# Performance work log

Measured on AMD Instinct MI355X. Metric: run time of the kernel, lower is better.

The kernel has to match this reference:

```python
import jax, jax.numpy as jnp
import numpy as np

B, N, T, D, H, E = 2, 1024, 8, 128, 4, 8192
DH = D // H
NEG_SLOPE = 0.2  # GATv2Conv default negative_slope


def _ln(x, g, b):
    m = jnp.mean(x, -1, keepdims=True)
    v = jnp.mean((x - m) ** 2, -1, keepdims=True)
    return (x - m) * jax.lax.rsqrt(v + 1e-5) * g + b


def _forward(x, edge_index, gat_wl, gat_wr, gat_att, gat_b, in_w, in_b, out_w, out_b,
             ffn_w1, ffn_b1, ffn_w2, ffn_b2, fus_w, fus_b,
             lns_g, lns_b, lnt1_g, lnt1_b, lnt2_g, lnt2_b, lnf_g, lnf_b):
    # ---- spatial branch: GATv2, vectorized over (B, T) instead of python loops ----
    loops = jnp.arange(N)
    src = jnp.concatenate([edge_index[0], loops])  # j: message source (PyG adds self loops)
    dst = jnp.concatenate([edge_index[1], loops])  # i: aggregation target
    xl = jnp.einsum('bntd,de->bnte', x, gat_wl).reshape(B, N, T, H, D)
    xr = jnp.einsum('bntd,de->bnte', x, gat_wr).reshape(B, N, T, H, D)
    ml = xl[:, src]                                  # [B,Et,T,H,D]
    mr = xr[:, dst]
    e = jax.nn.leaky_relu(ml + mr, NEG_SLOPE)
    logits = jnp.einsum('bethd,hd->beth', e, gat_att)
    logits = jnp.moveaxis(logits, 1, 0)              # [Et,B,T,H]
    mx = jax.ops.segment_max(logits, dst, num_segments=N)
    p = jnp.exp(logits - mx[dst])                    # stable edge softmax per dst node
    ssum = jax.ops.segment_sum(p, dst, num_segments=N)
    alpha = p / ssum[dst]                            # [Et,B,T,H]
    msg = alpha[..., None] * jnp.moveaxis(ml, 1, 0)
    agg = jax.ops.segment_sum(msg, dst, num_segments=N)  # [N,B,T,H,D]
    x_sp = jnp.moveaxis(agg.mean(3), 0, 1) + gat_b   # concat=False -> head mean; [B,N,T,D]
    x_sp = _ln(x_sp, lns_g, lns_b)

    # ---- temporal branch: MHA + FFN, vectorized over all B*N nodes ----
    xt = x.reshape(B * N, T, D)
    qkv = xt @ in_w + in_b
    q, k, v = jnp.split(qkv, 3, axis=-1)
    q = q.reshape(B * N, T, H, DH)
    k = k.reshape(B * N, T, H, DH)
    v = v.reshape(B * N, T, H, DH)
    scores = jnp.einsum('bthd,bshd->bhts', q, k) / np.float32(np.sqrt(DH))
    attn = jax.nn.softmax(scores, -1)
    o = jnp.einsum('bhts,bshd->bthd', attn, v).reshape(B * N, T, D)
    o = o @ out_w + out_b
    x1 = _ln(xt + o, lnt1_g, lnt1_b)
    ffn = jax.nn.gelu(x1 @ ffn_w1 + ffn_b1, approximate=False) @ ffn_w2 + ffn_b2
    x_tp = _ln(x1 + ffn, lnt2_g, lnt2_b).reshape(B, N, T, D)

    # ---- gated fusion with residual ----
    g = jax.nn.sigmoid(jnp.concatenate([x_sp, x_tp], -1) @ fus_w + fus_b)
    return _ln(g * x_sp + (1.0 - g) * x_tp + x, lnf_g, lnf_b)


def setup_inputs() -> dict:
    key = jax.random.key(0)
    ks = jax.random.split(key, 12)
    s = 0.05
    f = jnp.float32
    return {
        'x': jax.random.normal(ks[0], (B, N, T, D), f),
        'edge_index': jax.random.randint(ks[1], (2, E), 0, N),
        'gat_wl': jax.random.normal(ks[2], (D, H * D), f) * s,
        'gat_wr': jax.random.normal(ks[3], (D, H * D), f) * s,
        'gat_att': jax.random.normal(ks[4], (H, D), f) * s,
        'gat_b': jnp.zeros((D,), f),
        'in_w': jax.random.normal(ks[5], (D, 3 * D), f) * s,
        'in_b': jnp.zeros((3 * D,), f),
        'out_w': jax.random.normal(ks[6], (D, D), f) * s,
        'out_b': jnp.zeros((D,), f),
        'ffn_w1': jax.random.normal(ks[7], (D, 4 * D), f) * s,
        'ffn_b1': jnp.zeros((4 * D,), f),
        'ffn_w2': jax.random.normal(ks[8], (4 * D, D), f) * s,
        'ffn_b2': jnp.zeros((D,), f),
        'fus_w': jax.random.normal(ks[9], (2 * D, D), f) * s,
        'fus_b': jnp.zeros((D,), f),
        'lns_g': jnp.ones((D,), f), 'lns_b': jnp.zeros((D,), f),
        'lnt1_g': jnp.ones((D,), f), 'lnt1_b': jnp.zeros((D,), f),
        'lnt2_g': jnp.ones((D,), f), 'lnt2_b': jnp.zeros((D,), f),
        'lnf_g': jnp.ones((D,), f), 'lnf_b': jnp.zeros((D,), f),
    }


def reference(x, edge_index, gat_wl, gat_wr, gat_att, gat_b, in_w, in_b, out_w, out_b,
              ffn_w1, ffn_b1, ffn_w2, ffn_b2, fus_w, fus_b,
              lns_g, lns_b, lnt1_g, lnt1_b, lnt2_g, lnt2_b, lnf_g, lnf_b):
    return _forward(x, edge_index, gat_wl, gat_wr, gat_att, gat_b, in_w, in_b, out_w, out_b,
                    ffn_w1, ffn_b1, ffn_w2, ffn_b2, fus_w, fus_b,
                    lns_g, lns_b, lnt1_g, lnt1_b, lnt2_g, lnt2_b, lnf_g, lnf_b)
```

## Files before the change

kernel.cpp:

```cpp
#include <hip/hip_runtime.h>
#include <math.h>

#define B_ 2
#define N_ 1024
#define T_ 8
#define D_ 128
#define H_ 4
#define E_ 8192
#define EN_ 9216
#define M_ 16384

typedef unsigned short u16;
using bf16x8 = __attribute__((ext_vector_type(8))) short;
using f32x4  = __attribute__((ext_vector_type(4))) float;

__device__ __forceinline__ float bf2f(unsigned int u) {
  return __uint_as_float(u << 16);
}
__device__ __forceinline__ u16 f2bf(float f) {
  unsigned int x = __float_as_uint(f);
  x += 0x7fffu + ((x >> 16) & 1u);
  return (u16)(x >> 16);
}
__device__ __forceinline__ void load8f(const u16* p, float* f) {
  uint4 u = *(const uint4*)p;
  f[0]=bf2f(u.x & 0xffffu); f[1]=bf2f(u.x >> 16);
  f[2]=bf2f(u.y & 0xffffu); f[3]=bf2f(u.y >> 16);
  f[4]=bf2f(u.z & 0xffffu); f[5]=bf2f(u.z >> 16);
  f[6]=bf2f(u.w & 0xffffu); f[7]=bf2f(u.w >> 16);
}
__device__ __forceinline__ void gl2lds(const u16* g, u16* l) {
  __builtin_amdgcn_global_load_lds(
      (const __attribute__((address_space(1))) unsigned int*)(const void*)g,
      (__attribute__((address_space(3))) unsigned int*)(void*)l,
      16, 0, 0);
}

__global__ __launch_bounds__(256) void prep_k(const float* __restrict__ x,
                                              const float* __restrict__ wl,
                                              const float* __restrict__ wr,
                                              const float* __restrict__ inw,
                                              const float* __restrict__ outw,
                                              const float* __restrict__ f1,
                                              const float* __restrict__ f2,
                                              const float* __restrict__ fw,
                                              u16* __restrict__ XB,
                                              u16* __restrict__ WB) {
  int bi = blockIdx.x;
  if (bi < 2048) {
    int i = (bi * 256 + threadIdx.x) * 4;
    float4 v = *(const float4*)&x[i];
    u16 o[4] = {f2bf(v.x), f2bf(v.y), f2bf(v.z), f2bf(v.w)};
    *(ushort4*)&XB[i] = *(ushort4*)o;
    return;
  }
  int idx = (bi - 2048) * 256 + threadIdx.x;
  const float* src; int base, K, N;
  if      (idx < 65536)  { src = wl;   base = 0;      K = 128; N = 512; }
  else if (idx < 131072) { src = wr;   base = 65536;  K = 128; N = 512; }
  else if (idx < 180224) { src = inw;  base = 131072; K = 128; N = 384; }
  else if (idx < 196608) { src = outw; base = 180224; K = 128; N = 128; }
  else if (idx < 262144) { src = f1;   base = 196608; K = 128; N = 512; }
  else if (idx < 327680) { src = f2;   base = 262144; K = 512; N = 128; }
  else                   { src = fw;   base = 327680; K = 256; N = 128; }
  int o = idx - base;
  int n = o / K, k = o - n * K;
  WB[idx] = f2bf(src[k * N + n]);
}

__global__ __launch_bounds__(1024) void csr_k(const int* __restrict__ ei,
                                              int* __restrict__ offs,
                                              int* __restrict__ eids) {
  __shared__ int cnt[N_];
  __shared__ int cur[N_];
  int tid = threadIdx.x;
  cnt[tid] = 0;
  __syncthreads();
  for (int e = tid; e < EN_; e += 1024) {
    int d = (e < E_) ? ei[E_ + e] : (e - E_);
    atomicAdd(&cnt[d], 1);
  }
  __syncthreads();
  int mine = cnt[tid];
  for (int off = 1; off < 1024; off <<= 1) {
    int tv = (tid >= off) ? cnt[tid - off] : 0;
    __syncthreads();
    cnt[tid] += tv;
    __syncthreads();
  }
  int excl = cnt[tid] - mine;
  offs[tid] = excl;
  if (tid == 1023) offs[N_] = cnt[1023];
  cur[tid] = excl;
  __syncthreads();
  for (int e = tid; e < EN_; e += 1024) {
    int d = (e < E_) ? ei[E_ + e] : (e - E_);
    int pos = atomicAdd(&cur[d], 1);
    eids[pos] = e;
  }
}

template<int BM, int ACT, int ROUTE>
__global__ __launch_bounds__(256) void gemm_k(const u16* __restrict__ A, int lda,
                                              const u16* __restrict__ WT, int K,
                                              const float* __restrict__ bias,
                                              u16* __restrict__ C, int ldc,
                                              u16* __restrict__ R0,
                                              u16* __restrict__ R1,
                                              u16* __restrict__ R2,
                                              const float* __restrict__ b2) {
  constexpr int MI = BM / 32;
  __shared__ u16 As[BM * 32];
  __shared__ u16 Bs[128 * 32];
  int tid = threadIdx.x;
  int bx = blockIdx.x, by = blockIdx.y;
  int lane = tid & 63, wid = tid >> 6;
  int lr = lane & 15, lk = lane >> 4;
  int wm = (wid >> 1) * (BM / 2);
  int wn = (wid & 1) * 64;

  u16* Cb; int ldc_; int col0; const float* bias_;
  if (ROUTE) {
    if (bx < 4)      { Cb = R0; ldc_ = 512; col0 = bx * 128;       bias_ = nullptr; }
    else if (bx < 8) { Cb = R1; ldc_ = 512; col0 = (bx - 4) * 128; bias_ = nullptr; }
    else             { Cb = R2; ldc_ = 384; col0 = (bx - 8) * 128; bias_ = b2; }
  } else { Cb = C; ldc_ = ldc; col0 = bx * 128; bias_ = bias; }

  f32x4 acc[MI][4] = {};
  for (int k0 = 0; k0 < K; k0 += 32) {
    __syncthreads();
#pragma unroll
    for (int i = 0; i < BM / 64; ++i) {
      int o = tid * 16 + i * 4096;
      int row = o >> 6;
      int col = (o >> 1) & 31;
      gl2lds(A + (size_t)(by * BM + row) * lda + k0 + col,
             (u16*)((char*)As + wid * 1024 + i * 4096));
    }
#pragma unroll
    for (int i = 0; i < 2; ++i) {
      int o = tid * 16 + i * 4096;
      int nrow = o >> 6;
      int col = (o >> 1) & 31;
      gl2lds(WT + (size_t)(bx * 128 + nrow) * K + k0 + col,
             (u16*)((char*)Bs + wid * 1024 + i * 4096));
    }
    __syncthreads();
    bf16x8 bf[4];
#pragma unroll
    for (int ni = 0; ni < 4; ++ni)
      bf[ni] = *(const bf16x8*)&Bs[(wn + ni * 16 + lr) * 32 + lk * 8];
#pragma unroll
    for (int mi = 0; mi < MI; ++mi) {
      bf16x8 af = *(const bf16x8*)&As[(wm + mi * 16 + lr) * 32 + lk * 8];
#pragma unroll
      for (int ni = 0; ni < 4; ++ni)
        acc[mi][ni] = __builtin_amdgcn_mfma_f32_16x16x32_bf16(af, bf[ni], acc[mi][ni], 0, 0, 0);
    }
  }
  float bc[4];
#pragma unroll
  for (int ni = 0; ni < 4; ++ni)
    bc[ni] = bias_ ? bias_[col0 + wn + ni * 16 + lr] : 0.f;
#pragma unroll
  for (int mi = 0; mi < MI; ++mi) {
#pragma unroll
    for (int r = 0; r < 4; ++r) {
      int row = by * BM + wm + mi * 16 + lk * 4 + r;
#pragma unroll
      for (int ni = 0; ni < 4; ++ni) {
        int col = col0 + wn + ni * 16 + lr;
        float v = acc[mi][ni][r] + bc[ni];
        if (ACT) v = 0.5f * v * (1.f + erff(v * 0.70710678118f));
        Cb[(size_t)row * ldc_ + col] = f2bf(v);
      }
    }
  }
}

template<int EPI>
__global__ __launch_bounds__(256) void gemm_ln_k(const u16* __restrict__ A, int lda,
                                                 const u16* __restrict__ WT, int K,
                                                 const float* __restrict__ bias,
                                                 const float* __restrict__ xres,
                                                 const float* __restrict__ xsp,
                                                 const float* __restrict__ xtp,
                                                 const float* __restrict__ lng,
                                                 const float* __restrict__ lnb,
                                                 float* __restrict__ o32,
                                                 u16* __restrict__ o16, int os16) {
  __shared__ u16 As[64 * 32];
  __shared__ u16 Bs[128 * 32];
  __shared__ float rs[64][2], rq[64][2];
  int tid = threadIdx.x;
  int by = blockIdx.y;
  int lane = tid & 63, wid = tid >> 6;
  int lr = lane & 15, lk = lane >> 4;
  int wm = (wid >> 1) * 32, wn = (wid & 1) * 64;

  f32x4 acc[2][4] = {};
  for (int k0 = 0; k0 < K; k0 += 32) {
    __syncthreads();
    {
      int o = tid * 16;
      int row = o >> 6;
      int col = (o >> 1) & 31;
      gl2lds(A + (size_t)(by * 64 + row) * lda + k0 + col,
             (u16*)((char*)As + wid * 1024));
    }
#pragma unroll
    for (int i = 0; i < 2; ++i) {
      int o = tid * 16 + i * 4096;
      int nrow = o >> 6;
      int col = (o >> 1) & 31;
      gl2lds(WT + (size_t)nrow * K + k0 + col,
             (u16*)((char*)Bs + wid * 1024 + i * 4096));
    }
    __syncthreads();
    bf16x8 bf[4];
#pragma unroll
    for (int ni = 0; ni < 4; ++ni)
      bf[ni] = *(const bf16x8*)&Bs[(wn + ni * 16 + lr) * 32 + lk * 8];
#pragma unroll
    for (int mi = 0; mi < 2; ++mi) {
      bf16x8 af = *(const bf16x8*)&As[(wm + mi * 16 + lr) * 32 + lk * 8];
#pragma unroll
      for (int ni = 0; ni < 4; ++ni)
        acc[mi][ni] = __builtin_amdgcn_mfma_f32_16x16x32_bf16(af, bf[ni], acc[mi][ni], 0, 0, 0);
    }
  }
  float bc[4];
#pragma unroll
  for (int ni = 0; ni < 4; ++ni) bc[ni] = bias[wn + ni * 16 + lr];

#pragma unroll
  for (int mi = 0; mi < 2; ++mi) {
#pragma unroll
    for (int r = 0; r < 4; ++r) {
      int row = by * 64 + wm + mi * 16 + lk * 4 + r;
      float s = 0.f, s2 = 0.f;
#pragma unroll
      for (int ni = 0; ni < 4; ++ni) {
        int col = wn + ni * 16 + lr;
        float v = acc[mi][ni][r] + bc[ni];
        if (EPI == 1 || EPI == 2) {
          v += xres[(size_t)row * 128 + col];
        } else {
          float gg = 1.f / (1.f + expf(-v));
          v = gg * xsp[(size_t)row * 128 + col] + (1.f - gg) * xtp[(size_t)row * 128 + col]
              + xres[(size_t)row * 128 + col];
        }
        acc[mi][ni][r] = v;
        s += v; s2 += v * v;
      }
      s += __shfl_xor(s, 1, 64); s2 += __shfl_xor(s2, 1, 64);
      s += __shfl_xor(s, 2, 64); s2 += __shfl_xor(s2, 2, 64);
      s += __shfl_xor(s, 4, 64); s2 += __shfl_xor(s2, 4, 64);
      s += __shfl_xor(s, 8, 64); s2 += __shfl_xor(s2, 8, 64);
      if (lr == 0) {
        int rl = wm + mi * 16 + lk * 4 + r;
        rs[rl][wid & 1] = s;
        rq[rl][wid & 1] = s2;
      }
    }
  }
  __syncthreads();
#pragma unroll
  for (int mi = 0; mi < 2; ++mi) {
#pragma unroll
    for (int r = 0; r < 4; ++r) {
      int rl = wm + mi * 16 + lk * 4 + r;
      int row = by * 64 + rl;
      float tot = rs[rl][0] + rs[rl][1];
      float tq = rq[rl][0] + rq[rl][1];
      float mean = tot * (1.f / 128.f);
      float var = tq * (1.f / 128.f) - mean * mean;
      float rinv = rsqrtf(var + 1e-5f);
#pragma unroll
      for (int ni = 0; ni < 4; ++ni) {
        int col = wn + ni * 16 + lr;
        float o = (acc[mi][ni][r] - mean) * rinv * lng[col] + lnb[col];
        o32[(size_t)row * 128 + col] = o;
        if (EPI != 3) o16[(size_t)row * os16 + col] = f2bf(o);
      }
    }
  }
}

__global__ __launch_bounds__(64) void gat_fused_k(const u16* __restrict__ XL,
                                                  const u16* __restrict__ XR,
                                                  const int* __restrict__ offs,
                                                  const int* __restrict__ eids,
                                                  const int* __restrict__ ei,
                                                  const float* __restrict__ att,
                                                  const float* __restrict__ gb,
                                                  const float* __restrict__ lng,
                                                  const float* __restrict__ lnb,
                                                  float* __restrict__ XSP,
                                                  u16* __restrict__ XCAT) {
  int bid = blockIdx.x;
  int n = bid >> 4;
  int b = (bid >> 3) & 1;
  int t = bid & 7;
  int lane = threadIdx.x;
  int dd = (lane & 15) * 8;
  size_t tokn = (size_t)(b * N_ + n) * 8 + t;

  float mr[8], av[8];
  load8f(XR + tokn * 512 + lane * 8, mr);
  *(float4*)&av[0] = *(const float4*)(att + lane * 8);
  *(float4*)&av[4] = *(const float4*)(att + lane * 8 + 4);

  int beg = offs[n], end = offs[n + 1];
  float mH = -1e30f, sH = 0.f;
  float acc[8] = {0.f, 0.f, 0.f, 0.f, 0.f, 0.f, 0.f, 0.f};
  for (int i = beg; i < end; ++i) {
    int e = eids[i];
    int src = (e < E_) ? ei[e] : (e - E_);
    float ml[8];
    load8f(XL + ((size_t)(b * N_ + src) * 8 + t) * 512 + lane * 8, ml);
    float d = 0.f;
#pragma unroll
    for (int j = 0; j < 8; ++j) {
      float m = ml[j] + mr[j];
      m = (m > 0.f) ? m : 0.2f * m;
      d += m * av[j];
    }
    d += __shfl_xor(d, 1, 64);
    d += __shfl_xor(d, 2, 64);
    d += __shfl_xor(d, 4, 64);
    d += __shfl_xor(d, 8, 64);
    float mNew = fmaxf(mH, d);
    float scale = expf(mH - mNew);
    float p = expf(d - mNew);
    sH = sH * scale + p;
#pragma unroll
    for (int j = 0; j < 8; ++j) acc[j] = acc[j] * scale + p * ml[j];
    mH = mNew;
  }
  float invS = 1.f / sH;
#pragma unroll
  for (int j = 0; j < 8; ++j) acc[j] *= invS;
#pragma unroll
  for (int j = 0; j < 8; ++j) {
    acc[j] += __shfl_xor(acc[j], 16, 64);
    acc[j] += __shfl_xor(acc[j], 32, 64);
  }
#pragma unroll
  for (int j = 0; j < 8; ++j) acc[j] = acc[j] * 0.25f + gb[dd + j];
  float s = 0.f, s2 = 0.f;
#pragma unroll
  for (int j = 0; j < 8; ++j) { s += acc[j]; s2 += acc[j] * acc[j]; }
#pragma unroll
  for (int m = 1; m < 16; m <<= 1) {
    s += __shfl_xor(s, m, 64);
    s2 += __shfl_xor(s2, m, 64);
  }
  float mean = s * (1.f / 128.f);
  float var = s2 * (1.f / 128.f) - mean * mean;
  float r = rsqrtf(var + 1e-5f);
  if (lane < 16) {
    float o[8];
    u16 ob[8];
#pragma unroll
    for (int j = 0; j < 8; ++j) {
      o[j] = (acc[j] - mean) * r * lng[dd + j] + lnb[dd + j];
      ob[j] = f2bf(o[j]);
    }
    *(float4*)(XSP + tokn * 128 + dd)     = *(float4*)&o[0];
    *(float4*)(XSP + tokn * 128 + dd + 4) = *(float4*)&o[4];
    *(uint4*)&XCAT[tokn * 256 + dd] = *(uint4*)ob;
  }
}

__global__ __launch_bounds__(256) void attn_k(const u16* __restrict__ QKV,
                                              u16* __restrict__ OATT) {
  int pair = blockIdx.x * 4 + (threadIdx.x >> 6);
  int lane = threadIdx.x & 63;
  int bn = pair >> 2, h = pair & 3;
  int t = lane >> 3, s = lane & 7;
  const u16* base = QKV + (size_t)bn * 8 * 384;
  const u16* qp = base + t * 384 + h * 32;
  const u16* kp = base + s * 384 + 128 + h * 32;
  float sc = 0.f;
#pragma unroll
  for (int d0 = 0; d0 < 32; d0 += 8) {
    float q[8], k[8];
    load8f(qp + d0, q);
    load8f(kp + d0, k);
#pragma unroll
    for (int j = 0; j < 8; ++j) sc += q[j] * k[j];
  }
  sc *= 0.17677669529663687f;
  float m = sc;
  m = fmaxf(m, __shfl_xor(m, 1, 64));
  m = fmaxf(m, __shfl_xor(m, 2, 64));
  m = fmaxf(m, __shfl_xor(m, 4, 64));
  float p = expf(sc - m);
  float S = p;
  S += __shfl_xor(S, 1, 64);
  S += __shfl_xor(S, 2, 64);
  S += __shfl_xor(S, 4, 64);
  float alpha = p / S;
  int dg = lane & 7;
  int tbase = lane & 56;
  float o0 = 0.f, o1 = 0.f, o2 = 0.f, o3 = 0.f;
#pragma unroll
  for (int s2 = 0; s2 < 8; ++s2) {
    float a = __shfl(alpha, tbase + s2, 64);
    const u16* vp = base + s2 * 384 + 256 + h * 32 + dg * 4;
    o0 += a * bf2f(vp[0]);
    o1 += a * bf2f(vp[1]);
    o2 += a * bf2f(vp[2]);
    o3 += a * bf2f(vp[3]);
  }
  u16 ov[4] = {f2bf(o0), f2bf(o1), f2bf(o2), f2bf(o3)};
  *(ushort4*)&OATT[((size_t)bn * 8 + t) * 128 + h * 32 + dg * 4] = *(ushort4*)ov;
}

extern "C" void kernel_launch(void* const* d_in, const int* in_sizes, int n_in,
                              void* d_out, int out_size, void* d_ws, size_t ws_size,
                              hipStream_t stream) {
  const float* x       = (const float*)d_in[0];
  const int*   ei      = (const int*)d_in[1];
  const float* gat_att = (const float*)d_in[4];
  const float* gat_b   = (const float*)d_in[5];
  const float* in_b    = (const float*)d_in[7];
  const float* out_b   = (const float*)d_in[9];
  const float* ffn_b1  = (const float*)d_in[11];
  const float* ffn_b2  = (const float*)d_in[13];
  const float* fus_b   = (const float*)d_in[15];
  const float* lns_g   = (const float*)d_in[16];
  const float* lns_b   = (const float*)d_in[17];
  const float* lnt1_g  = (const float*)d_in[18];
  const float* lnt1_b  = (const float*)d_in[19];
  const float* lnt2_g  = (const float*)d_in[20];
  const float* lnt2_b  = (const float*)d_in[21];
  const float* lnf_g   = (const float*)d_in[22];
  const float* lnf_b   = (const float*)d_in[23];

  char* ws = (char*)d_ws;
  u16*   WB    = (u16*)ws;
  u16*   WT1   = WB;
  u16*   WTO   = WB + 180224;
  u16*   WTF1  = WB + 196608;
  u16*   WTF2  = WB + 262144;
  u16*   WTFUS = WB + 327680;
  int*   OFFS  = (int*)(ws + 3145728);
  int*   EIDS  = (int*)(ws + 3153920);
  u16*   XB   = (u16*)(ws + 4194304);
  u16*   OATT = XB;
  u16*   XL   = (u16*)(ws + 8388608);
  u16*   FFNH = XL;
  u16*   XR   = (u16*)(ws + 25165824);
  float* X1   = (float*)(ws + 33554432);
  u16*   QKV  = (u16*)(ws + 41943040);
  u16*   X1B  = (u16*)(ws + 41943040);
  float* XSP  = (float*)(ws + 54525952);
  u16*   XCAT = (u16*)(ws + 62914560);
  float* XTP  = (float*)(ws + 71303168);

  prep_k<<<dim3(3456), dim3(256), 0, stream>>>(x,
      (const float*)d_in[2], (const float*)d_in[3], (const float*)d_in[6],
      (const float*)d_in[8], (const float*)d_in[10], (const float*)d_in[12],
      (const float*)d_in[14], XB, WB);
  csr_k<<<dim3(1), dim3(1024), 0, stream>>>(ei, OFFS, EIDS);

  gemm_k<128,0,1><<<dim3(11, 128), dim3(256), 0, stream>>>(
      XB, 128, WT1, 128, nullptr, nullptr, 0, XL, XR, QKV, in_b);

  gat_fused_k<<<dim3(16384), dim3(64), 0, stream>>>(XL, XR, OFFS, EIDS, ei,
      gat_att, gat_b, lns_g, lns_b, XSP, XCAT);

  attn_k<<<dim3(2048), dim3(256), 0, stream>>>(QKV, OATT);
  gemm_ln_k<1><<<dim3(1, 256), dim3(256), 0, stream>>>(
      OATT, 128, WTO, 128, out_b, x, nullptr, nullptr, lnt1_g, lnt1_b, X1, X1B, 128);
  gemm_k<128,1,0><<<dim3(4, 128), dim3(256), 0, stream>>>(
      X1B, 128, WTF1, 128, ffn_b1, FFNH, 512, nullptr, nullptr, nullptr, nullptr);
  gemm_ln_k<2><<<dim3(1, 256), dim3(256), 0, stream>>>(
      FFNH, 512, WTF2, 512, ffn_b2, X1, nullptr, nullptr, lnt2_g, lnt2_b,
      XTP, XCAT + 128, 256);

  gemm_ln_k<3><<<dim3(1, 256), dim3(256), 0, stream>>>(
      XCAT, 256, WTFUS, 256, fus_b, x, XSP, XTP, lnf_g, lnf_b,
      (float*)d_out, nullptr, 0);
}
```

Baseline: 241.1 us.

## Merge prep with CSR build, fuse GAT with temporal attention, drop fp32 intermediates

Folds weight/input conversion and CSR construction into one launch, and runs the GAT aggregation and the temporal MHA as separate block ranges of a single kernel. The fp32 XSP/XTP buffers are removed, so the fusion epilogue reads the bf16 spatial and temporal branch values from XCAT. This cuts launch count and memory traffic, at the cost of lower precision in the gating inputs. The single CSR block now sits in a 601-block grid, which may leave it as a late straggler.

```diff
diff --git a/kernel.cpp b/kernel.cpp
--- a/kernel.cpp
+++ b/kernel.cpp
@@ -36,25 +36,9 @@
       16, 0, 0);
 }
 
-__global__ __launch_bounds__(256) void prep_k(const float* __restrict__ x,
-                                              const float* __restrict__ wl,
-                                              const float* __restrict__ wr,
-                                              const float* __restrict__ inw,
-                                              const float* __restrict__ outw,
-                                              const float* __restrict__ f1,
-                                              const float* __restrict__ f2,
-                                              const float* __restrict__ fw,
-                                              u16* __restrict__ XB,
-                                              u16* __restrict__ WB) {
-  int bi = blockIdx.x;
-  if (bi < 2048) {
-    int i = (bi * 256 + threadIdx.x) * 4;
-    float4 v = *(const float4*)&x[i];
-    u16 o[4] = {f2bf(v.x), f2bf(v.y), f2bf(v.z), f2bf(v.w)};
-    *(ushort4*)&XB[i] = *(ushort4*)o;
-    return;
-  }
-  int idx = (bi - 2048) * 256 + threadIdx.x;
+__device__ __forceinline__ u16 conv_w_elem(int idx,
+    const float* wl, const float* wr, const float* inw, const float* outw,
+    const float* f1, const float* f2, const float* fw) {
   const float* src; int base, K, N;
   if      (idx < 65536)  { src = wl;   base = 0;      K = 128; N = 512; }
   else if (idx < 131072) { src = wr;   base = 65536;  K = 128; N = 512; }
@@ -65,15 +49,34 @@
   else                   { src = fw;   base = 327680; K = 256; N = 128; }
   int o = idx - base;
   int n = o / K, k = o - n * K;
-  WB[idx] = f2bf(src[k * N + n]);
-}
-
-__global__ __launch_bounds__(1024) void csr_k(const int* __restrict__ ei,
-                                              int* __restrict__ offs,
-                                              int* __restrict__ eids) {
+  return f2bf(src[k * N + n]);
+}
+
+__global__ __launch_bounds__(1024) void prep_csr_k(const float* __restrict__ x,
+    const float* __restrict__ wl, const float* __restrict__ wr,
+    const float* __restrict__ inw, const float* __restrict__ outw,
+    const float* __restrict__ f1, const float* __restrict__ f2,
+    const float* __restrict__ fw,
+    u16* __restrict__ XB, u16* __restrict__ WB,
+    const int* __restrict__ ei, int* __restrict__ offs, int* __restrict__ eids) {
   __shared__ int cnt[N_];
   __shared__ int cur[N_];
+  int bi = blockIdx.x;
   int tid = threadIdx.x;
+  if (bi < 512) {
+    int i = (bi * 1024 + tid) * 4;
+    float4 v = *(const float4*)&x[i];
+    u16 o[4] = {f2bf(v.x), f2bf(v.y), f2bf(v.z), f2bf(v.w)};
+    *(ushort4*)&XB[i] = *(ushort4*)o;
+    return;
+  }
+  if (bi < 600) {
+    int base = (bi - 512) * 4096 + tid * 4;
+#pragma unroll
+    for (int j = 0; j < 4; ++j)
+      WB[base + j] = conv_w_elem(base + j, wl, wr, inw, outw, f1, f2, fw);
+    return;
+  }
   cnt[tid] = 0;
   __syncthreads();
   for (int e = tid; e < EN_; e += 1024) {
@@ -183,8 +186,7 @@
                                                  const u16* __restrict__ WT, int K,
                                                  const float* __restrict__ bias,
                                                  const float* __restrict__ xres,
-                                                 const float* __restrict__ xsp,
-                                                 const float* __restrict__ xtp,
+                                                 const u16* __restrict__ xcat,
                                                  const float* __restrict__ lng,
                                                  const float* __restrict__ lnb,
                                                  float* __restrict__ o32,
@@ -247,8 +249,9 @@
           v += xres[(size_t)row * 128 + col];
         } else {
           float gg = 1.f / (1.f + expf(-v));
-          v = gg * xsp[(size_t)row * 128 + col] + (1.f - gg) * xtp[(size_t)row * 128 + col]
-              + xres[(size_t)row * 128 + col];
+          float xsp = bf2f(xcat[(size_t)row * 256 + col]);
+          float xtp = bf2f(xcat[(size_t)row * 256 + 128 + col]);
+          v = gg * xsp + (1.f - gg) * xtp + xres[(size_t)row * 128 + col];
         }
         acc[mi][ni][r] = v;
         s += v; s2 += v * v;
@@ -280,14 +283,14 @@
       for (int ni = 0; ni < 4; ++ni) {
         int col = wn + ni * 16 + lr;
         float o = (acc[mi][ni][r] - mean) * rinv * lng[col] + lnb[col];
-        o32[(size_t)row * 128 + col] = o;
+        if (EPI != 2) o32[(size_t)row * 128 + col] = o;
         if (EPI != 3) o16[(size_t)row * os16 + col] = f2bf(o);
       }
     }
   }
 }
 
-__global__ __launch_bounds__(64) void gat_fused_k(const u16* __restrict__ XL,
+__global__ __launch_bounds__(256) void gat_attn_k(const u16* __restrict__ XL,
                                                   const u16* __restrict__ XR,
                                                   const int* __restrict__ offs,
                                                   const int* __restrict__ eids,
@@ -296,92 +299,88 @@
                                                   const float* __restrict__ gb,
                                                   const float* __restrict__ lng,
                                                   const float* __restrict__ lnb,
-                                                  float* __restrict__ XSP,
-                                                  u16* __restrict__ XCAT) {
+                                                  u16* __restrict__ XCAT,
+                                                  const u16* __restrict__ QKV,
+                                                  u16* __restrict__ OATT) {
   int bid = blockIdx.x;
-  int n = bid >> 4;
-  int b = (bid >> 3) & 1;
-  int t = bid & 7;
-  int lane = threadIdx.x;
-  int dd = (lane & 15) * 8;
-  size_t tokn = (size_t)(b * N_ + n) * 8 + t;
-
-  float mr[8], av[8];
-  load8f(XR + tokn * 512 + lane * 8, mr);
-  *(float4*)&av[0] = *(const float4*)(att + lane * 8);
-  *(float4*)&av[4] = *(const float4*)(att + lane * 8 + 4);
-
-  int beg = offs[n], end = offs[n + 1];
-  float mH = -1e30f, sH = 0.f;
-  float acc[8] = {0.f, 0.f, 0.f, 0.f, 0.f, 0.f, 0.f, 0.f};
-  for (int i = beg; i < end; ++i) {
-    int e = eids[i];
-    int src = (e < E_) ? ei[e] : (e - E_);
-    float ml[8];
-    load8f(XL + ((size_t)(b * N_ + src) * 8 + t) * 512 + lane * 8, ml);
-    float d = 0.f;
+  int wid = threadIdx.x >> 6;
+  int lane = threadIdx.x & 63;
+  if (bid < 4096) {
+    int w = bid * 4 + wid;
+    int n = w >> 4;
+    int b = (w >> 3) & 1;
+    int t = w & 7;
+    int dd = (lane & 15) * 8;
+    size_t tokn = (size_t)(b * N_ + n) * 8 + t;
+
+    float mr[8], av[8];
+    load8f(XR + tokn * 512 + lane * 8, mr);
+    *(float4*)&av[0] = *(const float4*)(att + lane * 8);
+    *(float4*)&av[4] = *(const float4*)(att + lane * 8 + 4);
+
+    int beg = offs[n], end = offs[n + 1];
+    float mH = -1e30f, sH = 0.f;
+    float acc[8] = {0.f, 0.f, 0.f, 0.f, 0.f, 0.f, 0.f, 0.f};
+    for (int i = beg; i < end; ++i) {
+      int e = eids[i];
+      int src = (e < E_) ? ei[e] : (e - E_);
+      float ml[8];
+      load8f(XL + ((size_t)(b * N_ + src) * 8 + t) * 512 + lane * 8, ml);
+      float d = 0.f;
+#pragma unroll
+      for (int j = 0; j < 8; ++j) {
+        float m = ml[j] + mr[j];
+        m = (m > 0.f) ? m : 0.2f * m;
+        d += m * av[j];
+      }
+      d += __shfl_xor(d, 1, 64);
+      d += __shfl_xor(d, 2, 64);
+      d += __shfl_xor(d, 4, 64);
+      d += __shfl_xor(d, 8, 64);
+      float mNew = fmaxf(mH, d);
+      float scale = expf(mH - mNew);
+      float p = expf(d - mNew);
+      sH = sH * scale + p;
+#pragma unroll
+      for (int j = 0; j < 8; ++j) acc[j] = acc[j] * scale + p * ml[j];
+      mH = mNew;
+    }
+    float invS = 1.f / sH;
+#pragma unroll
+    for (int j = 0; j < 8; ++j) acc[j] *= invS;
 #pragma unroll
     for (int j = 0; j < 8; ++j) {
-      float m = ml[j] + mr[j];
-      m = (m > 0.f) ? m : 0.2f * m;
-      d += m * av[j];
-    }
-    d += __shfl_xor(d, 1, 64);
-    d += __shfl_xor(d, 2, 64);
-    d += __shfl_xor(d, 4, 64);
-    d += __shfl_xor(d, 8, 64);
-    float mNew = fmaxf(mH, d);
-    float scale = expf(mH - mNew);
-    float p = expf(d - mNew);
-    sH = sH * scale + p;
-#pragma unroll
-    for (int j = 0; j < 8; ++j) acc[j] = acc[j] * scale + p * ml[j];
-    mH = mNew;
-  }
-  float invS = 1.f / sH;
-#pragma unroll
-  for (int j = 0; j < 8; ++j) acc[j] *= invS;
-#pragma unroll
-  for (int j = 0; j < 8; ++j) {
-    acc[j] += __shfl_xor(acc[j], 16, 64);
-    acc[j] += __shfl_xor(acc[j], 32, 64);
-  }
-#pragma unroll
-  for (int j = 0; j < 8; ++j) acc[j] = acc[j] * 0.25f + gb[dd + j];
-  float s = 0.f, s2 = 0.f;
-#pragma unroll
-  for (int j = 0; j < 8; ++j) { s += acc[j]; s2 += acc[j] * acc[j]; }
-#pragma unroll
-  for (int m = 1; m < 16; m <<= 1) {
-    s += __shfl_xor(s, m, 64);
-    s2 += __shfl_xor(s2, m, 64);
-  }
-  float mean = s * (1.f / 128.f);
-  float var = s2 * (1.f / 128.f) - mean * mean;
-  float r = rsqrtf(var + 1e-5f);
-  if (lane < 16) {
-    float o[8];
-    u16 ob[8];
-#pragma unroll
-    for (int j = 0; j < 8; ++j) {
-      o[j] = (acc[j] - mean) * r * lng[dd + j] + lnb[dd + j];
-      ob[j] = f2bf(o[j]);
-    }
-    *(float4*)(XSP + tokn * 128 + dd)     = *(float4*)&o[0];
-    *(float4*)(XSP + tokn * 128 + dd + 4) = *(float4*)&o[4];
-    *(uint4*)&XCAT[tokn * 256 + dd] = *(uint4*)ob;
-  }
-}
-
-__global__ __launch_bounds__(256) void attn_k(const u16* __restrict__ QKV,
-                                              u16* __restrict__ OATT) {
-  int pair = blockIdx.x * 4 + (threadIdx.x >> 6);
-  int lane = threadIdx.x & 63;
+      acc[j] += __shfl_xor(acc[j], 16, 64);
+      acc[j] += __shfl_xor(acc[j], 32, 64);
+    }
+#pragma unroll
+    for (int j = 0; j < 8; ++j) acc[j] = acc[j] * 0.25f + gb[dd + j];
+    float s = 0.f, s2 = 0.f;
+#pragma unroll
+    for (int j = 0; j < 8; ++j) { s += acc[j]; s2 += acc[j] * acc[j]; }
+#pragma unroll
+    for (int m = 1; m < 16; m <<= 1) {
+      s += __shfl_xor(s, m, 64);
+      s2 += __shfl_xor(s2, m, 64);
+    }
+    float mean = s * (1.f / 128.f);
+    float var = s2 * (1.f / 128.f) - mean * mean;
+    float r = rsqrtf(var + 1e-5f);
+    if (lane < 16) {
+      u16 ob[8];
+#pragma unroll
+      for (int j = 0; j < 8; ++j)
+        ob[j] = f2bf((acc[j] - mean) * r * lng[dd + j] + lnb[dd + j]);
+      *(uint4*)&XCAT[tokn * 256 + dd] = *(uint4*)ob;
+    }
+    return;
+  }
+  int pair = (bid - 4096) * 4 + wid;
   int bn = pair >> 2, h = pair & 3;
-  int t = lane >> 3, s = lane & 7;
+  int t = lane >> 3, sidx = lane & 7;
   const u16* base = QKV + (size_t)bn * 8 * 384;
   const u16* qp = base + t * 384 + h * 32;
-  const u16* kp = base + s * 384 + 128 + h * 32;
+  const u16* kp = base + sidx * 384 + 128 + h * 32;
   float sc = 0.f;
 #pragma unroll
   for (int d0 = 0; d0 < 32; d0 += 8) {
@@ -456,32 +455,30 @@
   float* X1   = (float*)(ws + 33554432);
   u16*   QKV  = (u16*)(ws + 41943040);
   u16*   X1B  = (u16*)(ws + 41943040);
-  float* XSP  = (float*)(ws + 54525952);
   u16*   XCAT = (u16*)(ws + 62914560);
-  float* XTP  = (float*)(ws + 71303168);
-
-  prep_k<<<dim3(3456), dim3(256), 0, stream>>>(x,
+
+  prep_csr_k<<<dim3(601), dim3(1024), 0, stream>>>(x,
       (const float*)d_in[2], (const float*)d_in[3], (const float*)d_in[6],
       (const float*)d_in[8], (const float*)d_in[10], (const float*)d_in[12],
-      (const float*)d_in[14], XB, WB);
-  csr_k<<<dim3(1), dim3(1024), 0, stream>>>(ei, OFFS, EIDS);
+      (const float*)d_in[14], XB, WB, ei, OFFS, EIDS);
 
   gemm_k<128,0,1><<<dim3(11, 128), dim3(256), 0, stream>>>(
       XB, 128, WT1, 128, nullptr, nullptr, 0, XL, XR, QKV, in_b);
 
-  gat_fused_k<<<dim3(16384), dim3(64), 0, stream>>>(XL, XR, OFFS, EIDS, ei,
-      gat_att, gat_b, lns_g, lns_b, XSP, XCAT);
-
-  attn_k<<<dim3(2048), dim3(256), 0, stream>>>(QKV, OATT);
+  gat_attn_k<<<dim3(6144), dim3(256), 0, stream>>>(XL, XR, OFFS, EIDS, ei,
+      gat_att, gat_b, lns_g, lns_b, XCAT, QKV, OATT);
+
   gemm_ln_k<1><<<dim3(1, 256), dim3(256), 0, stream>>>(
-      OATT, 128, WTO, 128, out_b, x, nullptr, nullptr, lnt1_g, lnt1_b, X1, X1B, 128);
+      OATT, 128, WTO, 128, out_b, x, nullptr, lnt1_g, lnt1_b, X1, X1B, 128);
+
   gemm_k<128,1,0><<<dim3(4, 128), dim3(256), 0, stream>>>(
       X1B, 128, WTF1, 128, ffn_b1, FFNH, 512, nullptr, nullptr, nullptr, nullptr);
+
   gemm_ln_k<2><<<dim3(1, 256), dim3(256), 0, stream>>>(
-      FFNH, 512, WTF2, 512, ffn_b2, X1, nullptr, nullptr, lnt2_g, lnt2_b,
-      XTP, XCAT + 128, 256);
+      FFNH, 512, WTF2, 512, ffn_b2, X1, nullptr, lnt2_g, lnt2_b,
+      nullptr, XCAT + 128, 256);
 
   gemm_ln_k<3><<<dim3(1, 256), dim3(256), 0, stream>>>(
-      XCAT, 256, WTFUS, 256, fus_b, x, XSP, XTP, lnf_g, lnf_b,
+      XCAT, 256, WTFUS, 256, fus_b, x, XCAT, lnf_g, lnf_b,
       (float*)d_out, nullptr, 0);
 }
```

Result: faster. 235.9 us (-2.2%).
